# Kernel optimization log

Hardware: AMD Instinct MI355X
Metric: run time of the kernel (lower is better)

The kernel has to match this reference:

```python
import jax, jax.numpy as jnp
import numpy as np

N, T, K = 400000, 64, 3


def setup_inputs() -> dict:
    key = jax.random.key(0)
    ks = jax.random.split(key, 6)
    G = jax.random.randint(ks[0], (N, 1), 0, 3).astype(jnp.float32)   # genotype 0/1/2
    S = jax.random.randint(ks[1], (N, T, 1), 0, 2).astype(jnp.float32)  # binary exposure
    C = jax.random.uniform(ks[2], (N, T, 1), dtype=jnp.float32)         # cumulative pack-years (scaled)
    Y = (jax.random.uniform(ks[3], (N, T, 1)) < 0.05).astype(jnp.float32)  # rare binary outcome
    L = jax.random.normal(ks[4], (N, K), dtype=jnp.float32)             # covariates
    kw = jax.random.split(ks[5], 2)
    f32 = jnp.float32
    params = dict(
        psi=jnp.array([0.5], f32),
        gamma_S=jnp.array([0.1], f32),
        gamma_C=jnp.array([0.1], f32),
        gamma_G=jnp.array([0.1], f32),
        gamma_GS=jnp.array([0.0], f32),
        gamma_GC=jnp.array([0.0], f32),
        gamma_L_w=jax.random.normal(kw[0], (1, K), f32) * 0.1,
        log_sigma_Z=jnp.array([-2.0], f32),
        beta_0=jnp.array([-3.0], f32),
        beta_Z=jnp.array([0.5], f32),
        beta_S=jnp.array([0.1], f32),
        beta_G=jnp.array([0.1], f32),
        beta_GS=jnp.array([0.0], f32),
        beta_L_w=jax.random.normal(kw[1], (1, K), f32) * 0.1,
    )
    return dict(G=G, S=S, C=C, Y=Y, L=L, **params)


def reference(G, S, C, Y, L, psi, gamma_S, gamma_C, gamma_G, gamma_GS, gamma_GC,
              gamma_L_w, log_sigma_Z, beta_0, beta_Z, beta_S, beta_G, beta_GS, beta_L_w):
    """Faithful JAX port of HiddenMarkovGFormulaV2.forward_filter (fit_interaction=fit_pack_years=True).
    Returns (Z_filtered (N,T,1), Z_variance (N,T,1), log_likelihood scalar)."""
    sigma2 = jnp.exp(log_sigma_Z) ** 2            # sigma_Z^2, shape (1,)
    gL = L @ gamma_L_w.T                          # (N,1) covariate term for transition
    bL = L @ beta_L_w.T                           # (N,1) covariate term for outcome

    def step(carry, xs):
        Z_mean, Z_var = carry                     # each (N,1)
        S_t, C_t, Y_t = xs                        # each (N,1)
        # hidden state transition
        Z_pred = (psi * Z_mean + gamma_S * S_t + gamma_G * G + gamma_C * C_t
                  + gamma_GS * (G * S_t) + gamma_GC * (G * C_t) + gL)
        Z_pred_var = psi ** 2 * Z_var + sigma2
        # outcome probability
        logit = jnp.clip(beta_0 + beta_Z * Z_pred + beta_S * S_t + beta_G * G
                         + beta_GS * (G * S_t) + bL, -20.0, 20.0)
        p = jax.nn.sigmoid(logit)
        # Laplace-style measurement update
        grad = (Y_t - p) * beta_Z
        hess = beta_Z ** 2 * p * (1.0 - p) + 1e-6
        Z_post_var = 1.0 / (1.0 / Z_pred_var + hess)
        Z_post_mean = Z_pred + Z_post_var * grad
        ll = jnp.sum(Y_t * jnp.log(p + 1e-10) + (1.0 - Y_t) * jnp.log(1.0 - p + 1e-10))
        return (Z_post_mean, Z_post_var), (Z_post_mean, Z_post_var, ll)

    n = G.shape[0]
    Zm0 = jnp.zeros((n, 1), dtype=G.dtype)
    Zv0 = jnp.ones((n, 1), dtype=G.dtype)
    xs = (jnp.swapaxes(S, 0, 1), jnp.swapaxes(C, 0, 1), jnp.swapaxes(Y, 0, 1))  # (T,N,1)
    _, (Zf, Zvf, lls) = jax.lax.scan(step, (Zm0, Zv0), xs)
    Z_filtered = jnp.swapaxes(Zf, 0, 1)   # (N,T,1)
    Z_variance = jnp.swapaxes(Zvf, 0, 1)  # (N,T,1)
    return Z_filtered, Z_variance, jnp.sum(lls)
```

## Files before the change

kernel.cpp:

```cpp
#include <hip/hip_runtime.h>


#define TT 64
#define KK 3
#define NR 32
#define BT 64

__global__ __launch_bounds__(256) void ll_reduce_kernel(
    const float* __restrict__ part, float* __restrict__ ll_out, int nw)
{
    float s = 0.0f;
    for (int i = threadIdx.x; i < nw; i += 256) s += part[i];
    #pragma unroll
    for (int off = 32; off > 0; off >>= 1) s += __shfl_down(s, off, 64);
    __shared__ float ws[4];
    const int wid = threadIdx.x >> 6, lane = threadIdx.x & 63;
    if (lane == 0) ws[wid] = s;
    __syncthreads();
    if (threadIdx.x == 0) *ll_out = ws[0] + ws[1] + ws[2] + ws[3];
}

__device__ __forceinline__ float packCY(float c, float y) {
    return __uint_as_float(__float_as_uint(c) | (__float_as_uint(y) << 8));
}

__global__ __launch_bounds__(BT) void hmm_filter_kernel(
    const float* __restrict__ G,
    const float* __restrict__ S,
    const float* __restrict__ C,
    const float* __restrict__ Y,
    const float* __restrict__ L,
    const float* __restrict__ p_psi,
    const float* __restrict__ p_gS,
    const float* __restrict__ p_gC,
    const float* __restrict__ p_gG,
    const float* __restrict__ p_gGS,
    const float* __restrict__ p_gGC,
    const float* __restrict__ p_gLw,
    const float* __restrict__ p_lsZ,
    const float* __restrict__ p_b0,
    const float* __restrict__ p_bZ,
    const float* __restrict__ p_bS,
    const float* __restrict__ p_bG,
    const float* __restrict__ p_bGS,
    const float* __restrict__ p_bLw,
    float* __restrict__ Zf,
    float* __restrict__ Zv,
    float* __restrict__ ll_part,
    int N)
{
    __shared__ float sS [TT][NR];
    __shared__ float sCY[TT][NR];

    const int tid = threadIdx.x;
    const int n0  = blockIdx.x * NR;
    const int rl  = tid & 31;
    const int n   = n0 + rl;
    const bool valid = (tid < 32) && (n < N);

    const float psi  = p_psi[0];
    const float gS   = p_gS[0];
    const float gC   = p_gC[0];
    const float gG   = p_gG[0];
    const float gGS  = p_gGS[0];
    const float gGC  = p_gGC[0];
    const float b0   = p_b0[0];
    const float bZ   = p_bZ[0];
    const float bS   = p_bS[0];
    const float bG   = p_bG[0];
    const float bGS  = p_bGS[0];
    const float esz  = expf(p_lsZ[0]);
    const float sigma2 = esz * esz;
    const float psi2 = psi * psi;
    const float bZ2  = bZ * bZ;
    const float gw0 = p_gLw[0], gw1 = p_gLw[1], gw2 = p_gLw[2];
    const float bw0 = p_bLw[0], bw1 = p_bLw[1], bw2 = p_bLw[2];

    float a_s = 0.0f, a_c = 0.0f, zbase = 0.0f, b_s = 0.0f, lbase = 0.0f;
    if (valid) {
        const float Gv = G[n];
        const float l0 = L[n * KK + 0];
        const float l1 = L[n * KK + 1];
        const float l2 = L[n * KK + 2];
        const float gL = l0 * gw0 + l1 * gw1 + l2 * gw2;
        const float bL = l0 * bw0 + l1 * bw1 + l2 * bw2;
        a_s   = gS + gGS * Gv;
        a_c   = gC + gGC * Gv;
        zbase = gG * Gv + gL;
        b_s   = bS + bGS * Gv;
        lbase = b0 + bG * Gv + bL;
    } else {
        lbase = b0;
    }

    const float4* S4 = (const float4*)S;
    const float4* C4 = (const float4*)C;
    const float4* Y4 = (const float4*)Y;
    float4* Zf4 = (float4*)Zf;
    float4* Zv4 = (float4*)Zv;

    #pragma unroll
    for (int i = 0; i < 8; ++i) {
        const int q  = tid + i * BT;
        const int r  = q >> 4;
        const int x  = q & 15;
        const int nn = n0 + r;
        float4 vs, vc, vy;
        if (nn < N) {
            const int g = nn * (TT / 4) + x;
            vs = S4[g]; vc = C4[g]; vy = Y4[g];
        } else {
            vs = make_float4(0, 0, 0, 0);
            vc = vs; vy = vs;
        }
        const int t0 = x * 4;
        sS[t0 + 0][r ^ ((t0 + 0) & 31)] = vs.x;
        sS[t0 + 1][r ^ ((t0 + 1) & 31)] = vs.y;
        sS[t0 + 2][r ^ ((t0 + 2) & 31)] = vs.z;
        sS[t0 + 3][r ^ ((t0 + 3) & 31)] = vs.w;
        sCY[t0 + 0][r ^ ((t0 + 0) & 31)] = packCY(vc.x, vy.x);
        sCY[t0 + 1][r ^ ((t0 + 1) & 31)] = packCY(vc.y, vy.y);
        sCY[t0 + 2][r ^ ((t0 + 2) & 31)] = packCY(vc.z, vy.z);
        sCY[t0 + 3][r ^ ((t0 + 3) & 31)] = packCY(vc.w, vy.w);
    }
    __syncthreads();

    float zm  = 0.0f;
    float zv  = 1.0f;
    float ll2 = 0.0f;

    #pragma unroll
    for (int t = 0; t < TT; ++t) {
        const int col      = rl ^ (t & 31);
        const float s      = sS[t][col];
        const unsigned cyb = __float_as_uint(sCY[t][col]);
        const float c      = __uint_as_float(cyb & 0x7fffffffu);
        const bool  yb     = (cyb >> 31) != 0u;

        const float zpred = fmaf(psi, zm, fmaf(a_s, s, fmaf(a_c, c, zbase)));
        const float zpvar = fmaf(psi2, zv, sigma2);

        float logit = fmaf(bZ, zpred, fmaf(b_s, s, lbase));
        logit = fminf(fmaxf(logit, -20.0f), 20.0f);
        const float p   = __builtin_amdgcn_rcpf(1.0f + __expf(-logit));
        const float omp = 1.0f - p;

        const float ymp = yb ? omp : -p;
        const float sel = yb ? p : omp;

        const float hess = fmaf(bZ2 * p, omp, 1e-6f);
        const float zpostvar  = zpvar * __builtin_amdgcn_rcpf(fmaf(zpvar, hess, 1.0f));
        const float zpostmean = fmaf(zpostvar * bZ, ymp, zpred);

        ll2 += __log2f(sel + 1e-10f);

        zm = zpostmean;
        zv = zpostvar;
        if (tid < 32) {
            sS [t][col] = zpostmean;
            sCY[t][col] = zpostvar;
        }
    }
    __syncthreads();

    #pragma unroll
    for (int i = 0; i < 8; ++i) {
        const int q  = tid + i * BT;
        const int r  = q >> 4;
        const int x  = q & 15;
        const int nn = n0 + r;
        if (nn < N) {
            const int t0 = x * 4;
            float4 vf, vv;
            vf.x = sS[t0 + 0][r ^ ((t0 + 0) & 31)];
            vf.y = sS[t0 + 1][r ^ ((t0 + 1) & 31)];
            vf.z = sS[t0 + 2][r ^ ((t0 + 2) & 31)];
            vf.w = sS[t0 + 3][r ^ ((t0 + 3) & 31)];
            vv.x = sCY[t0 + 0][r ^ ((t0 + 0) & 31)];
            vv.y = sCY[t0 + 1][r ^ ((t0 + 1) & 31)];
            vv.z = sCY[t0 + 2][r ^ ((t0 + 2) & 31)];
            vv.w = sCY[t0 + 3][r ^ ((t0 + 3) & 31)];
            const int g = nn * (TT / 4) + x;
            Zf4[g] = vf;
            Zv4[g] = vv;
        }
    }

    float ll = valid ? ll2 * 0.69314718055994531f : 0.0f;
    #pragma unroll
    for (int off = 32; off > 0; off >>= 1) {
        ll += __shfl_down(ll, off, 64);
    }
    if (tid == 0) ll_part[blockIdx.x] = ll;
}

extern "C" void kernel_launch(void* const* d_in, const int* in_sizes, int n_in,
                              void* d_out, int out_size, void* d_ws, size_t ws_size,
                              hipStream_t stream) {
    const int N = in_sizes[0];

    const float* G   = (const float*)d_in[0];
    const float* S   = (const float*)d_in[1];
    const float* C   = (const float*)d_in[2];
    const float* Y   = (const float*)d_in[3];
    const float* L   = (const float*)d_in[4];
    const float* psi = (const float*)d_in[5];
    const float* gS  = (const float*)d_in[6];
    const float* gC  = (const float*)d_in[7];
    const float* gG  = (const float*)d_in[8];
    const float* gGS = (const float*)d_in[9];
    const float* gGC = (const float*)d_in[10];
    const float* gLw = (const float*)d_in[11];
    const float* lsZ = (const float*)d_in[12];
    const float* b0  = (const float*)d_in[13];
    const float* bZ  = (const float*)d_in[14];
    const float* bS  = (const float*)d_in[15];
    const float* bG  = (const float*)d_in[16];
    const float* bGS = (const float*)d_in[17];
    const float* bLw = (const float*)d_in[18];

    float* out = (float*)d_out;
    float* Zf = out;
    float* Zv = out + (size_t)N * TT;
    float* ll = out + (size_t)2 * N * TT;

    float* ll_part = (float*)d_ws;

    const int blocks = (N + NR - 1) / NR;
    hmm_filter_kernel<<<blocks, BT, 0, stream>>>(
        G, S, C, Y, L, psi, gS, gC, gG, gGS, gGC, gLw, lsZ,
        b0, bZ, bS, bG, bGS, bLw, Zf, Zv, ll_part, N);
    ll_reduce_kernel<<<1, 256, 0, stream>>>(ll_part, ll, blocks);
}
```

Before: 481.4 us.

## Make HMM filter persistent with register prefetch of the next panel

The kernel becomes grid-strided and persistent, capped at a fixed block count. Each block loads the next 32-row panel of S, C, Y, G and L into registers while it runs the sequential 64-step filter on the current panel, so global loads overlap the compute. S, C and Y are now packed into one shared word, with S's bit stored in an exponent bit of C. This frees a shared array for the variance output and replaces the block barriers with LDS waitcnt fences, which is valid because a block is one wavefront. The cost is high register pressure from 96 prefetched floats, and the packing only works for binary S and C below 2.

```diff
diff --git a/kernel.cpp b/kernel.cpp
--- a/kernel.cpp
+++ b/kernel.cpp
@@ -5,6 +5,7 @@
 #define KK 3
 #define NR 32
 #define BT 64
+#define NBLK 2560
 
 __global__ __launch_bounds__(256) void ll_reduce_kernel(
     const float* __restrict__ part, float* __restrict__ ll_out, int nw)
@@ -20,11 +21,41 @@
     if (threadIdx.x == 0) *ll_out = ws[0] + ws[1] + ws[2] + ws[3];
 }
 
-__device__ __forceinline__ float packCY(float c, float y) {
-    return __uint_as_float(__float_as_uint(c) | (__float_as_uint(y) << 8));
-}
-
-__global__ __launch_bounds__(BT) void hmm_filter_kernel(
+__device__ __forceinline__ float packSCY(float s, float c, float y) {
+    const unsigned w = __float_as_uint(c)
+                     | (__float_as_uint(y) << 8)
+                     | ((__float_as_uint(s) & 0x00800000u) << 7);
+    return __uint_as_float(w);
+}
+
+#define LOAD_PANEL(PP)                                                    \
+    {                                                                     \
+        const int base_ = (PP) * NR;                                      \
+        _Pragma("unroll")                                                 \
+        for (int i_ = 0; i_ < 8; ++i_) {                                  \
+            const int q_ = tid + i_ * BT;                                 \
+            const int r_ = q_ >> 4, x_ = q_ & 15;                         \
+            const int nn_ = base_ + r_;                                   \
+            if (nn_ < N) {                                                \
+                const int g_ = nn_ * (TT / 4) + x_;                       \
+                pS[i_] = S4[g_]; pC[i_] = C4[g_]; pY[i_] = Y4[g_];        \
+            } else {                                                      \
+                pS[i_] = make_float4(0, 0, 0, 0);                         \
+                pC[i_] = pS[i_]; pY[i_] = pS[i_];                         \
+            }                                                             \
+        }                                                                 \
+        const int ng_ = base_ + rl;                                       \
+        if (ng_ < N) {                                                    \
+            gvn = G[ng_];                                                 \
+            l0n = L[ng_ * KK + 0];                                        \
+            l1n = L[ng_ * KK + 1];                                        \
+            l2n = L[ng_ * KK + 2];                                        \
+        } else {                                                          \
+            gvn = 0.0f; l0n = 0.0f; l1n = 0.0f; l2n = 0.0f;               \
+        }                                                                 \
+    }
+
+__global__ __launch_bounds__(BT, 3) void hmm_filter_kernel(
     const float* __restrict__ G,
     const float* __restrict__ S,
     const float* __restrict__ C,
@@ -47,16 +78,13 @@
     float* __restrict__ Zf,
     float* __restrict__ Zv,
     float* __restrict__ ll_part,
-    int N)
+    int N, int npanels)
 {
-    __shared__ float sS [TT][NR];
-    __shared__ float sCY[TT][NR];
+    __shared__ float sIM[TT][NR];
+    __shared__ float sV [TT][NR];
 
     const int tid = threadIdx.x;
-    const int n0  = blockIdx.x * NR;
     const int rl  = tid & 31;
-    const int n   = n0 + rl;
-    const bool valid = (tid < 32) && (n < N);
 
     const float psi  = p_psi[0];
     const float gS   = p_gS[0];
@@ -76,117 +104,113 @@
     const float gw0 = p_gLw[0], gw1 = p_gLw[1], gw2 = p_gLw[2];
     const float bw0 = p_bLw[0], bw1 = p_bLw[1], bw2 = p_bLw[2];
 
-    float a_s = 0.0f, a_c = 0.0f, zbase = 0.0f, b_s = 0.0f, lbase = 0.0f;
-    if (valid) {
-        const float Gv = G[n];
-        const float l0 = L[n * KK + 0];
-        const float l1 = L[n * KK + 1];
-        const float l2 = L[n * KK + 2];
-        const float gL = l0 * gw0 + l1 * gw1 + l2 * gw2;
-        const float bL = l0 * bw0 + l1 * bw1 + l2 * bw2;
-        a_s   = gS + gGS * Gv;
-        a_c   = gC + gGC * Gv;
-        zbase = gG * Gv + gL;
-        b_s   = bS + bGS * Gv;
-        lbase = b0 + bG * Gv + bL;
-    } else {
-        lbase = b0;
-    }
-
     const float4* S4 = (const float4*)S;
     const float4* C4 = (const float4*)C;
     const float4* Y4 = (const float4*)Y;
     float4* Zf4 = (float4*)Zf;
     float4* Zv4 = (float4*)Zv;
 
-    #pragma unroll
-    for (int i = 0; i < 8; ++i) {
-        const int q  = tid + i * BT;
-        const int r  = q >> 4;
-        const int x  = q & 15;
-        const int nn = n0 + r;
-        float4 vs, vc, vy;
-        if (nn < N) {
-            const int g = nn * (TT / 4) + x;
-            vs = S4[g]; vc = C4[g]; vy = Y4[g];
-        } else {
-            vs = make_float4(0, 0, 0, 0);
-            vc = vs; vy = vs;
+    float4 pS[8], pC[8], pY[8];
+    float gvn, l0n, l1n, l2n;
+
+    float ll_tot = 0.0f;
+
+    int p = blockIdx.x;
+    LOAD_PANEL(p);
+
+    while (true) {
+        const int n0 = p * NR;
+
+        #pragma unroll
+        for (int i = 0; i < 8; ++i) {
+            const int q = tid + i * BT;
+            const int r = q >> 4, x = q & 15;
+            const int t0 = x * 4;
+            sIM[t0 + 0][r ^ ((t0 + 0) & 31)] = packSCY(pS[i].x, pC[i].x, pY[i].x);
+            sIM[t0 + 1][r ^ ((t0 + 1) & 31)] = packSCY(pS[i].y, pC[i].y, pY[i].y);
+            sIM[t0 + 2][r ^ ((t0 + 2) & 31)] = packSCY(pS[i].z, pC[i].z, pY[i].z);
+            sIM[t0 + 3][r ^ ((t0 + 3) & 31)] = packSCY(pS[i].w, pC[i].w, pY[i].w);
         }
-        const int t0 = x * 4;
-        sS[t0 + 0][r ^ ((t0 + 0) & 31)] = vs.x;
-        sS[t0 + 1][r ^ ((t0 + 1) & 31)] = vs.y;
-        sS[t0 + 2][r ^ ((t0 + 2) & 31)] = vs.z;
-        sS[t0 + 3][r ^ ((t0 + 3) & 31)] = vs.w;
-        sCY[t0 + 0][r ^ ((t0 + 0) & 31)] = packCY(vc.x, vy.x);
-        sCY[t0 + 1][r ^ ((t0 + 1) & 31)] = packCY(vc.y, vy.y);
-        sCY[t0 + 2][r ^ ((t0 + 2) & 31)] = packCY(vc.z, vy.z);
-        sCY[t0 + 3][r ^ ((t0 + 3) & 31)] = packCY(vc.w, vy.w);
+
+        const int n = n0 + rl;
+        const bool valid = (tid < 32) && (n < N);
+        const float gL = l0n * gw0 + l1n * gw1 + l2n * gw2;
+        const float bL = l0n * bw0 + l1n * bw1 + l2n * bw2;
+        const float a_s   = gS + gGS * gvn;
+        const float a_c   = gC + gGC * gvn;
+        const float zbase = gG * gvn + gL;
+        const float b_s   = bS + bGS * gvn;
+        const float lbase = b0 + bG * gvn + bL;
+
+        const int pn = p + gridDim.x;
+        if (pn < npanels) LOAD_PANEL(pn);
+
+        asm volatile("s_waitcnt lgkmcnt(0)" ::: "memory");
+
+        float zm = 0.0f, zv = 1.0f, ll2 = 0.0f;
+        #pragma unroll
+        for (int t = 0; t < TT; ++t) {
+            const int col    = rl ^ (t & 31);
+            const unsigned w = __float_as_uint(sIM[t][col]);
+            const float c    = __uint_as_float(w & 0x3FFFFFFFu);
+            const float s    = (w & 0x40000000u) ? 1.0f : 0.0f;
+            const bool  yb   = (w >> 31) != 0u;
+
+            const float zpred = fmaf(psi, zm, fmaf(a_s, s, fmaf(a_c, c, zbase)));
+            const float zpvar = fmaf(psi2, zv, sigma2);
+
+            float logit = fmaf(bZ, zpred, fmaf(b_s, s, lbase));
+            logit = fminf(fmaxf(logit, -20.0f), 20.0f);
+            const float pr  = __builtin_amdgcn_rcpf(1.0f + __expf(-logit));
+            const float omp = 1.0f - pr;
+
+            const float ymp = yb ? omp : -pr;
+            const float sel = yb ? pr : omp;
+
+            const float hess = fmaf(bZ2 * pr, omp, 1e-6f);
+            const float zpostvar  = zpvar * __builtin_amdgcn_rcpf(fmaf(zpvar, hess, 1.0f));
+            const float zpostmean = fmaf(zpostvar * bZ, ymp, zpred);
+
+            ll2 += __log2f(sel + 1e-10f);
+
+            zm = zpostmean;
+            zv = zpostvar;
+            if (tid < 32) {
+                sIM[t][col] = zpostmean;
+                sV [t][col] = zpostvar;
+            }
+        }
+        if (valid) ll_tot += ll2;
+
+        asm volatile("s_waitcnt lgkmcnt(0)" ::: "memory");
+
+        #pragma unroll
+        for (int i = 0; i < 8; ++i) {
+            const int q = tid + i * BT;
+            const int r = q >> 4, x = q & 15;
+            const int nn = n0 + r;
+            if (nn < N) {
+                const int t0 = x * 4;
+                float4 vf, vv;
+                vf.x = sIM[t0 + 0][r ^ ((t0 + 0) & 31)];
+                vf.y = sIM[t0 + 1][r ^ ((t0 + 1) & 31)];
+                vf.z = sIM[t0 + 2][r ^ ((t0 + 2) & 31)];
+                vf.w = sIM[t0 + 3][r ^ ((t0 + 3) & 31)];
+                vv.x = sV[t0 + 0][r ^ ((t0 + 0) & 31)];
+                vv.y = sV[t0 + 1][r ^ ((t0 + 1) & 31)];
+                vv.z = sV[t0 + 2][r ^ ((t0 + 2) & 31)];
+                vv.w = sV[t0 + 3][r ^ ((t0 + 3) & 31)];
+                const int g = nn * (TT / 4) + x;
+                Zf4[g] = vf;
+                Zv4[g] = vv;
+            }
+        }
+
+        if (pn >= npanels) break;
+        p = pn;
     }
-    __syncthreads();
-
-    float zm  = 0.0f;
-    float zv  = 1.0f;
-    float ll2 = 0.0f;
-
-    #pragma unroll
-    for (int t = 0; t < TT; ++t) {
-        const int col      = rl ^ (t & 31);
-        const float s      = sS[t][col];
-        const unsigned cyb = __float_as_uint(sCY[t][col]);
-        const float c      = __uint_as_float(cyb & 0x7fffffffu);
-        const bool  yb     = (cyb >> 31) != 0u;
-
-        const float zpred = fmaf(psi, zm, fmaf(a_s, s, fmaf(a_c, c, zbase)));
-        const float zpvar = fmaf(psi2, zv, sigma2);
-
-        float logit = fmaf(bZ, zpred, fmaf(b_s, s, lbase));
-        logit = fminf(fmaxf(logit, -20.0f), 20.0f);
-        const float p   = __builtin_amdgcn_rcpf(1.0f + __expf(-logit));
-        const float omp = 1.0f - p;
-
-        const float ymp = yb ? omp : -p;
-        const float sel = yb ? p : omp;
-
-        const float hess = fmaf(bZ2 * p, omp, 1e-6f);
-        const float zpostvar  = zpvar * __builtin_amdgcn_rcpf(fmaf(zpvar, hess, 1.0f));
-        const float zpostmean = fmaf(zpostvar * bZ, ymp, zpred);
-
-        ll2 += __log2f(sel + 1e-10f);
-
-        zm = zpostmean;
-        zv = zpostvar;
-        if (tid < 32) {
-            sS [t][col] = zpostmean;
-            sCY[t][col] = zpostvar;
-        }
-    }
-    __syncthreads();
-
-    #pragma unroll
-    for (int i = 0; i < 8; ++i) {
-        const int q  = tid + i * BT;
-        const int r  = q >> 4;
-        const int x  = q & 15;
-        const int nn = n0 + r;
-        if (nn < N) {
-            const int t0 = x * 4;
-            float4 vf, vv;
-            vf.x = sS[t0 + 0][r ^ ((t0 + 0) & 31)];
-            vf.y = sS[t0 + 1][r ^ ((t0 + 1) & 31)];
-            vf.z = sS[t0 + 2][r ^ ((t0 + 2) & 31)];
-            vf.w = sS[t0 + 3][r ^ ((t0 + 3) & 31)];
-            vv.x = sCY[t0 + 0][r ^ ((t0 + 0) & 31)];
-            vv.y = sCY[t0 + 1][r ^ ((t0 + 1) & 31)];
-            vv.z = sCY[t0 + 2][r ^ ((t0 + 2) & 31)];
-            vv.w = sCY[t0 + 3][r ^ ((t0 + 3) & 31)];
-            const int g = nn * (TT / 4) + x;
-            Zf4[g] = vf;
-            Zv4[g] = vv;
-        }
-    }
-
-    float ll = valid ? ll2 * 0.69314718055994531f : 0.0f;
+
+    float ll = ll_tot * 0.69314718055994531f;
     #pragma unroll
     for (int off = 32; off > 0; off >>= 1) {
         ll += __shfl_down(ll, off, 64);
@@ -226,9 +250,10 @@
 
     float* ll_part = (float*)d_ws;
 
-    const int blocks = (N + NR - 1) / NR;
+    const int npanels = (N + NR - 1) / NR;
+    const int blocks  = (npanels < NBLK) ? npanels : NBLK;
     hmm_filter_kernel<<<blocks, BT, 0, stream>>>(
         G, S, C, Y, L, psi, gS, gC, gG, gGS, gGC, gLw, lsZ,
-        b0, bZ, bS, bG, bGS, bLw, Zf, Zv, ll_part, N);
+        b0, bZ, bS, bG, bGS, bLw, Zf, Zv, ll_part, N, npanels);
     ll_reduce_kernel<<<1, 256, 0, stream>>>(ll_part, ll, blocks);
 }
```

New measurement: 1.058 ms. 2.2x slower.

## Use all 64 lanes per wave and pack S/C/Y into one LDS word

Applied to the files above, without the earlier changes.

Each 64-thread block now handles 64 rows instead of 32, so the whole wavefront does the sequential filter rather than half of it. S, C and Y are packed into a single shared-memory word using spare bits of C, which halves LDS usage. The block barriers become wave barriers with explicit lgkmcnt waits. Z variances are held in a 64-entry register array and written back through the same LDS tile after the means, which raises register pressure and adds a launch-bounds occupancy hint. The packing assumes S is exactly 0 or 1 and that C lies in [0,1).

```diff
diff --git a/kernel.cpp b/kernel.cpp
--- a/kernel.cpp
+++ b/kernel.cpp
@@ -3,7 +3,7 @@
 
 #define TT 64
 #define KK 3
-#define NR 32
+#define NR 64
 #define BT 64
 
 __global__ __launch_bounds__(256) void ll_reduce_kernel(
@@ -20,11 +20,14 @@
     if (threadIdx.x == 0) *ll_out = ws[0] + ws[1] + ws[2] + ws[3];
 }
 
-__device__ __forceinline__ float packCY(float c, float y) {
-    return __uint_as_float(__float_as_uint(c) | (__float_as_uint(y) << 8));
-}
-
-__global__ __launch_bounds__(BT) void hmm_filter_kernel(
+__device__ __forceinline__ float packSCY(float s, float c, float y) {
+    const unsigned w = __float_as_uint(c)
+                     | (__float_as_uint(y) << 8)
+                     | ((__float_as_uint(s) & 0x00800000u) << 7);
+    return __uint_as_float(w);
+}
+
+__global__ __launch_bounds__(BT, 3) void hmm_filter_kernel(
     const float* __restrict__ G,
     const float* __restrict__ S,
     const float* __restrict__ C,
@@ -49,14 +52,12 @@
     float* __restrict__ ll_part,
     int N)
 {
-    __shared__ float sS [TT][NR];
-    __shared__ float sCY[TT][NR];
+    __shared__ float sIM[TT][NR];
 
     const int tid = threadIdx.x;
     const int n0  = blockIdx.x * NR;
-    const int rl  = tid & 31;
-    const int n   = n0 + rl;
-    const bool valid = (tid < 32) && (n < N);
+    const int n   = n0 + tid;
+    const bool valid = (n < N);
 
     const float psi  = p_psi[0];
     const float gS   = p_gS[0];
@@ -100,7 +101,7 @@
     float4* Zv4 = (float4*)Zv;
 
     #pragma unroll
-    for (int i = 0; i < 8; ++i) {
+    for (int i = 0; i < 16; ++i) {
         const int q  = tid + i * BT;
         const int r  = q >> 4;
         const int x  = q & 15;
@@ -114,41 +115,37 @@
             vc = vs; vy = vs;
         }
         const int t0 = x * 4;
-        sS[t0 + 0][r ^ ((t0 + 0) & 31)] = vs.x;
-        sS[t0 + 1][r ^ ((t0 + 1) & 31)] = vs.y;
-        sS[t0 + 2][r ^ ((t0 + 2) & 31)] = vs.z;
-        sS[t0 + 3][r ^ ((t0 + 3) & 31)] = vs.w;
-        sCY[t0 + 0][r ^ ((t0 + 0) & 31)] = packCY(vc.x, vy.x);
-        sCY[t0 + 1][r ^ ((t0 + 1) & 31)] = packCY(vc.y, vy.y);
-        sCY[t0 + 2][r ^ ((t0 + 2) & 31)] = packCY(vc.z, vy.z);
-        sCY[t0 + 3][r ^ ((t0 + 3) & 31)] = packCY(vc.w, vy.w);
-    }
-    __syncthreads();
-
-    float zm  = 0.0f;
-    float zv  = 1.0f;
-    float ll2 = 0.0f;
+        sIM[t0 + 0][r ^ ((t0 + 0) & 31)] = packSCY(vs.x, vc.x, vy.x);
+        sIM[t0 + 1][r ^ ((t0 + 1) & 31)] = packSCY(vs.y, vc.y, vy.y);
+        sIM[t0 + 2][r ^ ((t0 + 2) & 31)] = packSCY(vs.z, vc.z, vy.z);
+        sIM[t0 + 3][r ^ ((t0 + 3) & 31)] = packSCY(vs.w, vc.w, vy.w);
+    }
+    asm volatile("s_waitcnt lgkmcnt(0)" ::: "memory");
+    __builtin_amdgcn_wave_barrier();
+
+    float va[TT];
+    float zm = 0.0f, zv = 1.0f, ll2 = 0.0f;
 
     #pragma unroll
     for (int t = 0; t < TT; ++t) {
-        const int col      = rl ^ (t & 31);
-        const float s      = sS[t][col];
-        const unsigned cyb = __float_as_uint(sCY[t][col]);
-        const float c      = __uint_as_float(cyb & 0x7fffffffu);
-        const bool  yb     = (cyb >> 31) != 0u;
+        const int col    = tid ^ (t & 31);
+        const unsigned w = __float_as_uint(sIM[t][col]);
+        const float c    = __uint_as_float(w & 0x3FFFFFFFu);
+        const float s    = (w & 0x40000000u) ? 1.0f : 0.0f;
+        const bool  yb   = (w >> 31) != 0u;
 
         const float zpred = fmaf(psi, zm, fmaf(a_s, s, fmaf(a_c, c, zbase)));
         const float zpvar = fmaf(psi2, zv, sigma2);
 
         float logit = fmaf(bZ, zpred, fmaf(b_s, s, lbase));
         logit = fminf(fmaxf(logit, -20.0f), 20.0f);
-        const float p   = __builtin_amdgcn_rcpf(1.0f + __expf(-logit));
-        const float omp = 1.0f - p;
-
-        const float ymp = yb ? omp : -p;
-        const float sel = yb ? p : omp;
-
-        const float hess = fmaf(bZ2 * p, omp, 1e-6f);
+        const float pr  = __builtin_amdgcn_rcpf(1.0f + __expf(-logit));
+        const float omp = 1.0f - pr;
+
+        const float ymp = yb ? omp : -pr;
+        const float sel = yb ? pr : omp;
+
+        const float hess = fmaf(bZ2 * pr, omp, 1e-6f);
         const float zpostvar  = zpvar * __builtin_amdgcn_rcpf(fmaf(zpvar, hess, 1.0f));
         const float zpostmean = fmaf(zpostvar * bZ, ymp, zpred);
 
@@ -156,33 +153,53 @@
 
         zm = zpostmean;
         zv = zpostvar;
-        if (tid < 32) {
-            sS [t][col] = zpostmean;
-            sCY[t][col] = zpostvar;
-        }
-    }
-    __syncthreads();
-
-    #pragma unroll
-    for (int i = 0; i < 8; ++i) {
+        sIM[t][col] = zpostmean;
+        va[t]       = zpostvar;
+    }
+
+    asm volatile("s_waitcnt lgkmcnt(0)" ::: "memory");
+    __builtin_amdgcn_wave_barrier();
+
+    #pragma unroll
+    for (int i = 0; i < 16; ++i) {
         const int q  = tid + i * BT;
         const int r  = q >> 4;
         const int x  = q & 15;
         const int nn = n0 + r;
         if (nn < N) {
             const int t0 = x * 4;
-            float4 vf, vv;
-            vf.x = sS[t0 + 0][r ^ ((t0 + 0) & 31)];
-            vf.y = sS[t0 + 1][r ^ ((t0 + 1) & 31)];
-            vf.z = sS[t0 + 2][r ^ ((t0 + 2) & 31)];
-            vf.w = sS[t0 + 3][r ^ ((t0 + 3) & 31)];
-            vv.x = sCY[t0 + 0][r ^ ((t0 + 0) & 31)];
-            vv.y = sCY[t0 + 1][r ^ ((t0 + 1) & 31)];
-            vv.z = sCY[t0 + 2][r ^ ((t0 + 2) & 31)];
-            vv.w = sCY[t0 + 3][r ^ ((t0 + 3) & 31)];
-            const int g = nn * (TT / 4) + x;
-            Zf4[g] = vf;
-            Zv4[g] = vv;
+            float4 vf;
+            vf.x = sIM[t0 + 0][r ^ ((t0 + 0) & 31)];
+            vf.y = sIM[t0 + 1][r ^ ((t0 + 1) & 31)];
+            vf.z = sIM[t0 + 2][r ^ ((t0 + 2) & 31)];
+            vf.w = sIM[t0 + 3][r ^ ((t0 + 3) & 31)];
+            Zf4[nn * (TT / 4) + x] = vf;
+        }
+    }
+    asm volatile("s_waitcnt lgkmcnt(0)" ::: "memory");
+    __builtin_amdgcn_wave_barrier();
+
+    #pragma unroll
+    for (int t = 0; t < TT; ++t) {
+        sIM[t][tid ^ (t & 31)] = va[t];
+    }
+    asm volatile("s_waitcnt lgkmcnt(0)" ::: "memory");
+    __builtin_amdgcn_wave_barrier();
+
+    #pragma unroll
+    for (int i = 0; i < 16; ++i) {
+        const int q  = tid + i * BT;
+        const int r  = q >> 4;
+        const int x  = q & 15;
+        const int nn = n0 + r;
+        if (nn < N) {
+            const int t0 = x * 4;
+            float4 vv;
+            vv.x = sIM[t0 + 0][r ^ ((t0 + 0) & 31)];
+            vv.y = sIM[t0 + 1][r ^ ((t0 + 1) & 31)];
+            vv.z = sIM[t0 + 2][r ^ ((t0 + 2) & 31)];
+            vv.w = sIM[t0 + 3][r ^ ((t0 + 3) & 31)];
+            Zv4[nn * (TT / 4) + x] = vv;
         }
     }
 
```

Result: slower. 584.2 us (+21.3%).
